# Performance work log

Measured on AMD Instinct MI355X. Metric: run time of the kernel, lower is better.

## Reference

```python
import jax, jax.numpy as jnp
import numpy as np
import math


def setup_inputs() -> dict:
    key = jax.random.key(0)
    kq, kk, kv = jax.random.split(key, 3)
    B, N, H = 4, 4096, 128
    return {
        "q": jax.random.normal(kq, (B, N, H), dtype=jnp.float32),
        "k": jax.random.normal(kk, (B, N, H), dtype=jnp.float32),
        "v": jax.random.normal(kv, (B, N, H), dtype=jnp.float32),
        "block_size": 128,
    }


def reference(q, k, v, block_size):
    # The torch module is an exact online-softmax (flash-attention) tiling of
    # full, unmasked softmax attention: out = softmax(q k^T / sqrt(H)) @ v.
    # The block-wise m/l running updates compute the identical result, so the
    # clean dense form below is the faithful math.
    H = q.shape[-1]
    scale = 1.0 / math.sqrt(H)
    s = jnp.einsum("bnh,bmh->bnm", q, k) * scale  # [B, N, N]
    p = jax.nn.softmax(s, axis=-1)                 # numerically stable softmax
    return jnp.einsum("bnm,bmh->bnh", p, v)
```

## Files before the change

kernel.cpp:

```cpp
#include <hip/hip_runtime.h>

typedef __attribute__((ext_vector_type(4))) float f32x4;
typedef __attribute__((ext_vector_type(8))) short short8;

#define DEVI static __device__ __forceinline__

constexpr int B_ = 4;
constexpr int N_ = 4096;
constexpr int H_ = 128;
constexpr size_t ELEMS = (size_t)B_ * N_ * H_;
constexpr size_t TSB = ELEMS * 2;

constexpr int QT = 128;
constexpr int KVB = 64;
constexpr int NTH = 256;

DEVI unsigned short f2bf(float x) {
  union { float f; unsigned u; } a; a.f = x;
  unsigned u = a.u;
  return (unsigned short)((u + 0x7FFFu + ((u >> 16) & 1u)) >> 16);
}

DEVI int swz(int byteoff, int row) { return byteoff ^ ((row & 7) << 4); }

DEVI void gl_lds16(const void* g, void* l) {
  __builtin_amdgcn_global_load_lds(
      (const __attribute__((address_space(1))) void*)g,
      (__attribute__((address_space(3))) void*)l, 16, 0, 0);
}

__global__ void conv_qk(const float* __restrict__ q, const float* __restrict__ k,
                        unsigned short* __restrict__ qb, unsigned short* __restrict__ kb) {
  const float qscale = 0.08838834764831845f * 1.4426950408889634f;
  size_t i = (size_t)blockIdx.x * blockDim.x + threadIdx.x;
  {
    const float4* s = (const float4*)q + 2 * i;
    float4 a = s[0], b = s[1];
    short8 t;
    t[0] = (short)f2bf(a.x * qscale); t[1] = (short)f2bf(a.y * qscale);
    t[2] = (short)f2bf(a.z * qscale); t[3] = (short)f2bf(a.w * qscale);
    t[4] = (short)f2bf(b.x * qscale); t[5] = (short)f2bf(b.y * qscale);
    t[6] = (short)f2bf(b.z * qscale); t[7] = (short)f2bf(b.w * qscale);
    *(short8*)(qb + i * 8) = t;
  }
  {
    const float4* s = (const float4*)k + 2 * i;
    float4 a = s[0], b = s[1];
    short8 t;
    t[0] = (short)f2bf(a.x); t[1] = (short)f2bf(a.y);
    t[2] = (short)f2bf(a.z); t[3] = (short)f2bf(a.w);
    t[4] = (short)f2bf(b.x); t[5] = (short)f2bf(b.y);
    t[6] = (short)f2bf(b.z); t[7] = (short)f2bf(b.w);
    *(short8*)(kb + i * 8) = t;
  }
}

__global__ void conv_vt(const float* __restrict__ v, unsigned short* __restrict__ vt) {
  __shared__ unsigned short T[64][72];
  const int n0 = blockIdx.x * 64, h0 = blockIdx.y * 64, b = blockIdx.z;
  const int t = threadIdx.x;
  const int c4 = t & 15, r = t >> 4;
#pragma unroll
  for (int i = 0; i < 4; ++i) {
    int n = n0 + r + 16 * i;
    float4 val = *(const float4*)(v + ((size_t)b * N_ + n) * H_ + h0 + 4 * c4);
    T[4 * c4 + 0][r + 16 * i] = f2bf(val.x);
    T[4 * c4 + 1][r + 16 * i] = f2bf(val.y);
    T[4 * c4 + 2][r + 16 * i] = f2bf(val.z);
    T[4 * c4 + 3][r + 16 * i] = f2bf(val.w);
  }
  __syncthreads();
  const int c8 = t & 7, hr = t >> 3;
#pragma unroll
  for (int i = 0; i < 2; ++i) {
    int hl = hr + 32 * i;
    short8 val = *(const short8*)(&T[hl][8 * c8]);
    *(short8*)(vt + ((size_t)b * H_ + h0 + hl) * N_ + n0 + 8 * c8) = val;
  }
}

template <int KS>
__global__ __launch_bounds__(NTH, 2)
void fattn_v4(const unsigned short* __restrict__ qws,
              const unsigned short* __restrict__ kws,
              const unsigned short* __restrict__ vtws,
              float* __restrict__ opart, float* __restrict__ mlpart) {
  constexpr int KVRANGE = N_ / KS;
  constexpr int NST = KVRANGE / KVB;

  __shared__ __align__(16) char smem[73728];
  char* Kb0 = smem;
  char* Vb0 = smem + 32768;

  const int tid = threadIdx.x, wave = tid >> 6, lane = tid & 63;
  const int l15 = lane & 15, l4 = lane >> 4;
  const int b = blockIdx.y, z = blockIdx.z;
  const int qg0 = blockIdx.x * QT + wave * 32;
  const size_t kvz = (size_t)z * KVRANGE;
  const int swzm = (l15 & 7) << 4;
  char* Pw = smem + 65536 + wave * 2048;

  const unsigned short* qp0 = qws + ((size_t)b * N_ + qg0 + l15) * H_;
  short8 qf0[4], qf1[4];
#pragma unroll
  for (int kc = 0; kc < 4; ++kc) {
    qf0[kc] = *(const short8*)(qp0 + 8 * l4 + 32 * kc);
    qf1[kc] = *(const short8*)(qp0 + 16 * H_ + 8 * l4 + 32 * kc);
  }

  f32x4 O0[8], O1[8];
#pragma unroll
  for (int i = 0; i < 8; ++i) { O0[i] = (f32x4){0,0,0,0}; O1[i] = (f32x4){0,0,0,0}; }
  float m0 = -__builtin_inff(), l0 = 0.f, m1 = -__builtin_inff(), l1 = 0.f;

  const char* kbase = (const char*)(kws + ((size_t)b * N_ + kvz) * H_);
  const char* vbase = (const char*)(vtws + (size_t)b * H_ * N_) + kvz * 2;

  auto stage = [&](int buf, int step) {
    const char* kt = kbase + (size_t)step * KVB * H_ * 2;
    char* kd = Kb0 + buf * 16384;
#pragma unroll
    for (int i = 0; i < 4; ++i) {
      int off = (tid + 256 * i) * 16;
      int row = off >> 8, col = off & 255;
      gl_lds16(kt + row * 256 + (col ^ ((row & 7) << 4)), kd + off);
    }
    const char* vt0 = vbase + (size_t)step * KVB * 2;
    char* vd = Vb0 + buf * 16384;
#pragma unroll
    for (int i = 0; i < 4; ++i) {
      int off = (tid + 256 * i) * 16;
      int h = off >> 7, colb = off & 127;
      gl_lds16(vt0 + (size_t)h * (N_ * 2) + (colb ^ ((h & 7) << 4)), vd + off);
    }
  };

  auto softmax_prep = [&](f32x4 (&S)[4], float& m, float& l, f32x4 (&O)[8], short8 (&pf)[2]) {
    float mx = S[0][0];
#pragma unroll
    for (int ct = 0; ct < 4; ++ct)
#pragma unroll
      for (int r = 0; r < 4; ++r) mx = fmaxf(mx, S[ct][r]);
    mx = fmaxf(mx, __shfl_xor(mx, 16));
    mx = fmaxf(mx, __shfl_xor(mx, 32));
    float mi = fmaxf(m, mx);
    float alpha = __builtin_amdgcn_exp2f(m - mi);
    m = mi;
    float rs = 0.f;
    uint2 pk[4];
#pragma unroll
    for (int ct = 0; ct < 4; ++ct) {
      float p0 = __builtin_amdgcn_exp2f(S[ct][0] - mi);
      float p1 = __builtin_amdgcn_exp2f(S[ct][1] - mi);
      float p2 = __builtin_amdgcn_exp2f(S[ct][2] - mi);
      float p3 = __builtin_amdgcn_exp2f(S[ct][3] - mi);
      rs += (p0 + p1) + (p2 + p3);
      pk[ct].x = (unsigned)f2bf(p0) | ((unsigned)f2bf(p1) << 16);
      pk[ct].y = (unsigned)f2bf(p2) | ((unsigned)f2bf(p3) << 16);
    }
    rs += __shfl_xor(rs, 16);
    rs += __shfl_xor(rs, 32);
    l = l * alpha + rs;
#pragma unroll
    for (int i = 0; i < 8; ++i) O[i] = O[i] * alpha;
#pragma unroll
    for (int ct = 0; ct < 4; ++ct)
      *(uint2*)(Pw + ((l15 * 128 + 32 * ct + 8 * l4) ^ swzm)) = pk[ct];
    pf[0] = *(const short8*)(Pw + ((l15 * 128 + 16 * l4) ^ swzm));
    pf[1] = *(const short8*)(Pw + ((l15 * 128 + 16 * l4 + 64) ^ swzm));
  };

  stage(0, 0);
  __syncthreads();
  int cur = 0;

  for (int st = 0; st < NST; ++st) {
    if (st + 1 < NST) stage(cur ^ 1, st + 1);

    const char* Kl = Kb0 + cur * 16384;
    const char* Vl = Vb0 + cur * 16384;

    f32x4 S0[4], S1[4];
#pragma unroll
    for (int ct = 0; ct < 4; ++ct) { S0[ct] = (f32x4){0,0,0,0}; S1[ct] = (f32x4){0,0,0,0}; }
    __builtin_amdgcn_s_setprio(1);
#pragma unroll
    for (int ct = 0; ct < 4; ++ct) {
      int kr = 16 * ct + l15;
#pragma unroll
      for (int kc = 0; kc < 4; ++kc) {
        short8 af = *(const short8*)(Kl + ((kr * 256 + 16 * l4 + 64 * kc) ^ ((kr & 7) << 4)));
        S0[ct] = __builtin_amdgcn_mfma_f32_16x16x32_bf16(af, qf0[kc], S0[ct], 0, 0, 0);
        S1[ct] = __builtin_amdgcn_mfma_f32_16x16x32_bf16(af, qf1[kc], S1[ct], 0, 0, 0);
      }
    }
    __builtin_amdgcn_s_setprio(0);

    short8 pf0[2], pf1[2];
    softmax_prep(S0, m0, l0, O0, pf0);
    softmax_prep(S1, m1, l1, O1, pf1);

    __builtin_amdgcn_s_setprio(1);
#pragma unroll
    for (int ct2 = 0; ct2 < 8; ++ct2) {
      int hr = 16 * ct2 + l15;
#pragma unroll
      for (int kc2 = 0; kc2 < 2; ++kc2) {
        short8 vf = *(const short8*)(Vl + ((hr * 128 + 16 * l4 + 64 * kc2) ^ ((hr & 7) << 4)));
        O0[ct2] = __builtin_amdgcn_mfma_f32_16x16x32_bf16(vf, pf0[kc2], O0[ct2], 0, 0, 0);
        O1[ct2] = __builtin_amdgcn_mfma_f32_16x16x32_bf16(vf, pf1[kc2], O1[ct2], 0, 0, 0);
      }
    }
    __builtin_amdgcn_s_setprio(0);

    __syncthreads();
    cur ^= 1;
  }

#pragma unroll
  for (int ct2 = 0; ct2 < 8; ++ct2) {
    int q0 = wave * 32 + l15;
    *(f32x4*)(smem + q0 * 512 + ((64 * ct2 + 16 * l4) ^ ((q0 & 7) << 4))) = O0[ct2];
    int q1 = q0 + 16;
    *(f32x4*)(smem + q1 * 512 + ((64 * ct2 + 16 * l4) ^ ((q1 & 7) << 4))) = O1[ct2];
  }
  if (l4 == 0) {
    size_t r0 = ((size_t)z * B_ + b) * N_ + qg0 + l15;
    mlpart[2 * r0] = m0;
    mlpart[2 * r0 + 1] = l0;
    mlpart[2 * (r0 + 16)] = m1;
    mlpart[2 * (r0 + 16) + 1] = l1;
  }
  __syncthreads();
  float* od = opart + (((size_t)z * B_ + b) * N_ + (size_t)blockIdx.x * QT) * H_;
#pragma unroll
  for (int i = 0; i < 16; ++i) {
    int off = (tid + 256 * i) * 16;
    int q = off >> 9, colb = off & 511;
    f32x4 val = *(const f32x4*)(smem + q * 512 + (colb ^ ((q & 7) << 4)));
    *(f32x4*)((char*)od + (size_t)q * 512 + colb) = val;
  }
}

template <int KS>
__global__ void combine_k(const float* __restrict__ opart, const float* __restrict__ mlpart,
                          float* __restrict__ out) {
  const int t = threadIdx.x;
  size_t row = (size_t)blockIdx.x * 8 + (t >> 5);
  int hc = (t & 31) * 4;
  float mz[KS], lz[KS];
  float mi = -__builtin_inff();
#pragma unroll
  for (int z = 0; z < KS; ++z) {
    size_t r = (size_t)z * B_ * N_ + row;
    mz[z] = mlpart[2 * r];
    lz[z] = mlpart[2 * r + 1];
    mi = fmaxf(mi, mz[z]);
  }
  float lsum = 0.f;
  float az[KS];
#pragma unroll
  for (int z = 0; z < KS; ++z) {
    az[z] = __builtin_amdgcn_exp2f(mz[z] - mi);
    lsum += az[z] * lz[z];
  }
  float rinv = 1.f / lsum;
  f32x4 acc = (f32x4){0, 0, 0, 0};
#pragma unroll
  for (int z = 0; z < KS; ++z) {
    f32x4 oz = *(const f32x4*)(opart + (size_t)z * B_ * N_ * H_ + row * H_ + hc);
    acc = acc + oz * (az[z] * rinv);
  }
  *(f32x4*)(out + row * H_ + hc) = acc;
}

constexpr int FB_QTILE = 64;
constexpr int FB_KVSTEP = 128;
constexpr int FB_KVHALF = 64;
constexpr int FB_NTH = 512;
constexpr int FB_NSTEPS = N_ / FB_KVSTEP;

__global__ __launch_bounds__(FB_NTH, 2)
void fattn_fast(const unsigned short* __restrict__ qws,
                const unsigned short* __restrict__ kws,
                const unsigned short* __restrict__ vtws,
                float* __restrict__ out) {
  __shared__ unsigned short Kbuf[2][FB_KVSTEP * H_];
  __shared__ unsigned short Vbuf[2][H_ * FB_KVSTEP];
  __shared__ unsigned short Plds[8][16 * FB_KVHALF];
  __shared__ float MLlds[4][16][2];

  const int tid = threadIdx.x;
  const int wave = tid >> 6;
  const int lane = tid & 63;
  const int l15 = lane & 15;
  const int l4 = lane >> 4;
  const int sub = wave & 3;
  const int grp = wave >> 2;

  const int b = blockIdx.y;
  const int qbase = blockIdx.x * FB_QTILE;

  const unsigned short* qp = qws + ((size_t)b * N_ + qbase + sub * 16 + l15) * H_;
  short8 qfrag[4];
#pragma unroll
  for (int kc = 0; kc < 4; ++kc)
    qfrag[kc] = *(const short8*)(qp + 8 * l4 + 32 * kc);

  f32x4 Oacc[8];
#pragma unroll
  for (int i = 0; i < 8; ++i) Oacc[i] = (f32x4){0.f, 0.f, 0.f, 0.f};
  float mrun[4], lrun[4];
#pragma unroll
  for (int r = 0; r < 4; ++r) { mrun[r] = -__builtin_inff(); lrun[r] = 0.f; }

  const char* kbase = (const char*)(kws + (size_t)b * N_ * H_);
  const char* vbase = (const char*)(vtws + (size_t)b * H_ * N_);
  const int kvbase = grp * FB_KVHALF;
  char* pbase = (char*)Plds[wave];

  auto stage = [&](int buf, int step) {
    const char* ktile = kbase + (size_t)step * FB_KVSTEP * H_ * 2;
#pragma unroll
    for (int i = 0; i < 4; ++i) {
      int chunk = wave * 4 + i;
      int off = chunk * 1024 + lane * 16;
      int row = off >> 8, col = off & 255;
      gl_lds16(ktile + row * 256 + (col ^ ((row & 7) << 4)),
               (char*)Kbuf[buf] + chunk * 1024);
    }
#pragma unroll
    for (int i = 0; i < 4; ++i) {
      int chunk = wave * 4 + i;
      int h = chunk * 4 + (lane >> 4);
      int colb = (lane & 15) * 16;
      gl_lds16(vbase + (size_t)h * (N_ * 2) + (size_t)step * 256 + (colb ^ ((h & 7) << 4)),
               (char*)Vbuf[buf] + chunk * 1024);
    }
  };

  int cur = 0;
  stage(0, 0);
  __syncthreads();

  for (int step = 0; step < FB_NSTEPS; ++step) {
    if (step + 1 < FB_NSTEPS) stage(cur ^ 1, step + 1);

    const char* Kl = (const char*)Kbuf[cur];
    const char* Vl = (const char*)Vbuf[cur];

    f32x4 S[4];
#pragma unroll
    for (int ct = 0; ct < 4; ++ct) S[ct] = (f32x4){0.f, 0.f, 0.f, 0.f};
#pragma unroll
    for (int ct = 0; ct < 4; ++ct) {
      int kvrow = kvbase + ct * 16 + l15;
#pragma unroll
      for (int kc = 0; kc < 4; ++kc) {
        short8 bfrag = *(const short8*)(Kl +
            swz(kvrow * 256 + (8 * l4 + 32 * kc) * 2, kvrow));
        S[ct] = __builtin_amdgcn_mfma_f32_16x16x32_bf16(qfrag[kc], bfrag, S[ct], 0, 0, 0);
      }
    }

    float mnew[4];
#pragma unroll
    for (int r = 0; r < 4; ++r) {
      float mx = fmaxf(fmaxf(S[0][r], S[1][r]), fmaxf(S[2][r], S[3][r]));
      mx = fmaxf(mx, __shfl_xor(mx, 1));
      mx = fmaxf(mx, __shfl_xor(mx, 2));
      mx = fmaxf(mx, __shfl_xor(mx, 4));
      mx = fmaxf(mx, __shfl_xor(mx, 8));
      mnew[r] = mx;
    }
    float alpha[4];
#pragma unroll
    for (int r = 0; r < 4; ++r) {
      float mi = fmaxf(mrun[r], mnew[r]);
      alpha[r] = __builtin_amdgcn_exp2f(mrun[r] - mi);
      mrun[r] = mi;
    }
    float rsum[4] = {0.f, 0.f, 0.f, 0.f};
    unsigned short pb[4][4];
#pragma unroll
    for (int ct = 0; ct < 4; ++ct)
#pragma unroll
      for (int r = 0; r < 4; ++r) {
        float pv = __builtin_amdgcn_exp2f(S[ct][r] - mrun[r]);
        rsum[r] += pv;
        pb[ct][r] = f2bf(pv);
      }
#pragma unroll
    for (int r = 0; r < 4; ++r) {
      float s = rsum[r];
      s += __shfl_xor(s, 1); s += __shfl_xor(s, 2);
      s += __shfl_xor(s, 4); s += __shfl_xor(s, 8);
      lrun[r] = lrun[r] * alpha[r] + s;
    }
#pragma unroll
    for (int ct2 = 0; ct2 < 8; ++ct2)
#pragma unroll
      for (int r = 0; r < 4; ++r) Oacc[ct2][r] *= alpha[r];

#pragma unroll
    for (int ct = 0; ct < 4; ++ct)
#pragma unroll
      for (int r = 0; r < 4; ++r) {
        int qrow = 4 * l4 + r;
        int kv = l15 + 16 * ct;
        *(unsigned short*)(pbase + swz(qrow * 128 + kv * 2, qrow)) = pb[ct][r];
      }

#pragma unroll
    for (int kc2 = 0; kc2 < 2; ++kc2) {
      short8 afrag = *(const short8*)(pbase +
          swz(l15 * 128 + (8 * l4 + 32 * kc2) * 2, l15));
#pragma unroll
      for (int ct2 = 0; ct2 < 8; ++ct2) {
        int h = l15 + 16 * ct2;
        short8 bfrag = *(const short8*)(Vl +
            swz(h * 256 + (kvbase + 8 * l4 + 32 * kc2) * 2, h));
        Oacc[ct2] = __builtin_amdgcn_mfma_f32_16x16x32_bf16(afrag, bfrag, Oacc[ct2], 0, 0, 0);
      }
    }

    __syncthreads();
    cur ^= 1;
  }

  __syncthreads();
  float* mergeO = (float*)Kbuf;
  if (grp == 1) {
#pragma unroll
    for (int ct2 = 0; ct2 < 8; ++ct2)
#pragma unroll
      for (int r = 0; r < 4; ++r) {
        int qrow = 4 * l4 + r, h = l15 + 16 * ct2;
        mergeO[(sub * 16 + qrow) * H_ + h] = Oacc[ct2][r];
      }
    if (l15 == 0) {
#pragma unroll
      for (int r = 0; r < 4; ++r) {
        int qrow = 4 * l4 + r;
        MLlds[sub][qrow][0] = mrun[r];
        MLlds[sub][qrow][1] = lrun[r];
      }
    }
  }
  __syncthreads();
  if (grp == 0) {
    float aA[4], aB[4], rl[4];
#pragma unroll
    for (int r = 0; r < 4; ++r) {
      int qrow = 4 * l4 + r;
      float mB = MLlds[sub][qrow][0], lB = MLlds[sub][qrow][1];
      float mi = fmaxf(mrun[r], mB);
      aA[r] = __builtin_amdgcn_exp2f(mrun[r] - mi);
      aB[r] = __builtin_amdgcn_exp2f(mB - mi);
      rl[r] = 1.f / (lrun[r] * aA[r] + lB * aB[r]);
    }
    float* outp = out + ((size_t)b * N_ + qbase + sub * 16) * H_;
#pragma unroll
    for (int ct2 = 0; ct2 < 8; ++ct2)
#pragma unroll
      for (int r = 0; r < 4; ++r) {
        int qrow = 4 * l4 + r, h = l15 + 16 * ct2;
        float ob = mergeO[(sub * 16 + qrow) * H_ + h];
        outp[(size_t)qrow * H_ + h] = (Oacc[ct2][r] * aA[r] + ob * aB[r]) * rl[r];
      }
  }
}

extern "C" void kernel_launch(void* const* d_in, const int* in_sizes, int n_in,
                              void* d_out, int out_size, void* d_ws, size_t ws_size,
                              hipStream_t stream) {
  const float* q = (const float*)d_in[0];
  const float* k = (const float*)d_in[1];
  const float* v = (const float*)d_in[2];
  float* out = (float*)d_out;

  auto need = [](int ks) {
    return 3 * TSB + (size_t)ks * ELEMS * 4 + (size_t)ks * B_ * N_ * 2 * 4;
  };

  if (ws_size >= need(4)) {
    unsigned short* qb = (unsigned short*)d_ws;
    unsigned short* kb = qb + ELEMS;
    unsigned short* vt = kb + ELEMS;
    float* opart = (float*)((char*)d_ws + 3 * TSB);
    float* mlpart = opart + (size_t)4 * ELEMS;
    conv_qk<<<dim3((unsigned)(ELEMS / 8 / 256)), dim3(256), 0, stream>>>(q, k, qb, kb);
    conv_vt<<<dim3(N_ / 64, H_ / 64, B_), dim3(256), 0, stream>>>(v, vt);
    fattn_v4<4><<<dim3(N_ / QT, B_, 4), dim3(NTH), 0, stream>>>(qb, kb, vt, opart, mlpart);
    combine_k<4><<<dim3(B_ * N_ / 8), dim3(256), 0, stream>>>(opart, mlpart, out);
  } else if (ws_size >= need(2)) {
    unsigned short* qb = (unsigned short*)d_ws;
    unsigned short* kb = qb + ELEMS;
    unsigned short* vt = kb + ELEMS;
    float* opart = (float*)((char*)d_ws + 3 * TSB);
    float* mlpart = opart + (size_t)2 * ELEMS;
    conv_qk<<<dim3((unsigned)(ELEMS / 8 / 256)), dim3(256), 0, stream>>>(q, k, qb, kb);
    conv_vt<<<dim3(N_ / 64, H_ / 64, B_), dim3(256), 0, stream>>>(v, vt);
    fattn_v4<2><<<dim3(N_ / QT, B_, 2), dim3(NTH), 0, stream>>>(qb, kb, vt, opart, mlpart);
    combine_k<2><<<dim3(B_ * N_ / 8), dim3(256), 0, stream>>>(opart, mlpart, out);
  } else if (ws_size >= 3 * TSB) {
    unsigned short* qb = (unsigned short*)d_ws;
    unsigned short* kb = qb + ELEMS;
    unsigned short* vt = kb + ELEMS;
    conv_qk<<<dim3((unsigned)(ELEMS / 8 / 256)), dim3(256), 0, stream>>>(q, k, qb, kb);
    conv_vt<<<dim3(N_ / 64, H_ / 64, B_), dim3(256), 0, stream>>>(v, vt);
    fattn_fast<<<dim3(N_ / FB_QTILE, B_), dim3(FB_NTH), 0, stream>>>(qb, kb, vt, out);
  }
}
```

Baseline: 73.54 us.

## Use lazy softmax rescaling, remap grid to 1D for XCD locality, reorder MFMA loops

```diff
diff --git a/kernel.cpp b/kernel.cpp
--- a/kernel.cpp
+++ b/kernel.cpp
@@ -81,7 +81,7 @@
 
 template <int KS>
 __global__ __launch_bounds__(NTH, 2)
-void fattn_v4(const unsigned short* __restrict__ qws,
+void fattn_v5(const unsigned short* __restrict__ qws,
               const unsigned short* __restrict__ kws,
               const unsigned short* __restrict__ vtws,
               float* __restrict__ opart, float* __restrict__ mlpart) {
@@ -94,8 +94,22 @@
 
   const int tid = threadIdx.x, wave = tid >> 6, lane = tid & 63;
   const int l15 = lane & 15, l4 = lane >> 4;
-  const int b = blockIdx.y, z = blockIdx.z;
-  const int qg0 = blockIdx.x * QT + wave * 32;
+
+  const int bid = blockIdx.x;
+  int x, b, z;
+  if (KS == 4) {
+    int pair = (bid & 7) * 2 + ((bid >> 3) & 1);
+    x = bid >> 4;
+    b = pair >> 2;
+    z = pair & 3;
+  } else {
+    int pair = bid & 7;
+    x = bid >> 3;
+    b = pair >> 1;
+    z = pair & 1;
+  }
+
+  const int qg0 = x * QT + wave * 32;
   const size_t kvz = (size_t)z * KVRANGE;
   const int swzm = (l15 & 7) << 4;
   char* Pw = smem + 65536 + wave * 2048;
@@ -111,7 +125,7 @@
   f32x4 O0[8], O1[8];
 #pragma unroll
   for (int i = 0; i < 8; ++i) { O0[i] = (f32x4){0,0,0,0}; O1[i] = (f32x4){0,0,0,0}; }
-  float m0 = -__builtin_inff(), l0 = 0.f, m1 = -__builtin_inff(), l1 = 0.f;
+  float m0 = 0.f, l0 = 0.f, m1 = 0.f, l1 = 0.f;
 
   const char* kbase = (const char*)(kws + ((size_t)b * N_ + kvz) * H_);
   const char* vbase = (const char*)(vtws + (size_t)b * H_ * N_) + kvz * 2;
@@ -136,36 +150,46 @@
   };
 
   auto softmax_prep = [&](f32x4 (&S)[4], float& m, float& l, f32x4 (&O)[8], short8 (&pf)[2]) {
-    float mx = S[0][0];
+    float p[16];
 #pragma unroll
     for (int ct = 0; ct < 4; ++ct)
 #pragma unroll
-      for (int r = 0; r < 4; ++r) mx = fmaxf(mx, S[ct][r]);
+      for (int r = 0; r < 4; ++r)
+        p[4 * ct + r] = __builtin_amdgcn_exp2f(S[ct][r] - m);
+    float a0 = fmaxf(p[0], p[1]), a1 = fmaxf(p[2], p[3]);
+    float a2 = fmaxf(p[4], p[5]), a3 = fmaxf(p[6], p[7]);
+    float a4 = fmaxf(p[8], p[9]), a5 = fmaxf(p[10], p[11]);
+    float a6 = fmaxf(p[12], p[13]), a7 = fmaxf(p[14], p[15]);
+    float b0 = fmaxf(a0, a1), b1 = fmaxf(a2, a3), b2 = fmaxf(a4, a5), b3 = fmaxf(a6, a7);
+    float mx = fmaxf(fmaxf(b0, b1), fmaxf(b2, b3));
     mx = fmaxf(mx, __shfl_xor(mx, 16));
     mx = fmaxf(mx, __shfl_xor(mx, 32));
-    float mi = fmaxf(m, mx);
-    float alpha = __builtin_amdgcn_exp2f(m - mi);
-    m = mi;
-    float rs = 0.f;
-    uint2 pk[4];
-#pragma unroll
-    for (int ct = 0; ct < 4; ++ct) {
-      float p0 = __builtin_amdgcn_exp2f(S[ct][0] - mi);
-      float p1 = __builtin_amdgcn_exp2f(S[ct][1] - mi);
-      float p2 = __builtin_amdgcn_exp2f(S[ct][2] - mi);
-      float p3 = __builtin_amdgcn_exp2f(S[ct][3] - mi);
-      rs += (p0 + p1) + (p2 + p3);
-      pk[ct].x = (unsigned)f2bf(p0) | ((unsigned)f2bf(p1) << 16);
-      pk[ct].y = (unsigned)f2bf(p2) | ((unsigned)f2bf(p3) << 16);
-    }
+    float s0 = (p[0] + p[1]) + (p[2] + p[3]);
+    float s1 = (p[4] + p[5]) + (p[6] + p[7]);
+    float s2 = (p[8] + p[9]) + (p[10] + p[11]);
+    float s3 = (p[12] + p[13]) + (p[14] + p[15]);
+    float rs = (s0 + s1) + (s2 + s3);
     rs += __shfl_xor(rs, 16);
     rs += __shfl_xor(rs, 32);
-    l = l * alpha + rs;
-#pragma unroll
-    for (int i = 0; i < 8; ++i) O[i] = O[i] * alpha;
-#pragma unroll
-    for (int ct = 0; ct < 4; ++ct)
-      *(uint2*)(Pw + ((l15 * 128 + 32 * ct + 8 * l4) ^ swzm)) = pk[ct];
+    if (__builtin_expect(!__all(mx <= 256.f), 0)) {
+      float sc = fmaxf(mx, 1.f);
+      float ai = 1.f / sc;
+      m += __builtin_amdgcn_logf(sc);
+      l = (l + rs) * ai;
+#pragma unroll
+      for (int i = 0; i < 16; ++i) p[i] *= ai;
+#pragma unroll
+      for (int i = 0; i < 8; ++i) O[i] = O[i] * ai;
+    } else {
+      l += rs;
+    }
+#pragma unroll
+    for (int ct = 0; ct < 4; ++ct) {
+      uint2 pk;
+      pk.x = (unsigned)f2bf(p[4 * ct]) | ((unsigned)f2bf(p[4 * ct + 1]) << 16);
+      pk.y = (unsigned)f2bf(p[4 * ct + 2]) | ((unsigned)f2bf(p[4 * ct + 3]) << 16);
+      *(uint2*)(Pw + ((l15 * 128 + 32 * ct + 8 * l4) ^ swzm)) = pk;
+    }
     pf[0] = *(const short8*)(Pw + ((l15 * 128 + 16 * l4) ^ swzm));
     pf[1] = *(const short8*)(Pw + ((l15 * 128 + 16 * l4 + 64) ^ swzm));
   };
@@ -185,10 +209,10 @@
     for (int ct = 0; ct < 4; ++ct) { S0[ct] = (f32x4){0,0,0,0}; S1[ct] = (f32x4){0,0,0,0}; }
     __builtin_amdgcn_s_setprio(1);
 #pragma unroll
-    for (int ct = 0; ct < 4; ++ct) {
-      int kr = 16 * ct + l15;
-#pragma unroll
-      for (int kc = 0; kc < 4; ++kc) {
+    for (int kc = 0; kc < 4; ++kc) {
+#pragma unroll
+      for (int ct = 0; ct < 4; ++ct) {
+        int kr = 16 * ct + l15;
         short8 af = *(const short8*)(Kl + ((kr * 256 + 16 * l4 + 64 * kc) ^ ((kr & 7) << 4)));
         S0[ct] = __builtin_amdgcn_mfma_f32_16x16x32_bf16(af, qf0[kc], S0[ct], 0, 0, 0);
         S1[ct] = __builtin_amdgcn_mfma_f32_16x16x32_bf16(af, qf1[kc], S1[ct], 0, 0, 0);
@@ -202,10 +226,10 @@
 
     __builtin_amdgcn_s_setprio(1);
 #pragma unroll
-    for (int ct2 = 0; ct2 < 8; ++ct2) {
-      int hr = 16 * ct2 + l15;
-#pragma unroll
-      for (int kc2 = 0; kc2 < 2; ++kc2) {
+    for (int kc2 = 0; kc2 < 2; ++kc2) {
+#pragma unroll
+      for (int ct2 = 0; ct2 < 8; ++ct2) {
+        int hr = 16 * ct2 + l15;
         short8 vf = *(const short8*)(Vl + ((hr * 128 + 16 * l4 + 64 * kc2) ^ ((hr & 7) << 4)));
         O0[ct2] = __builtin_amdgcn_mfma_f32_16x16x32_bf16(vf, pf0[kc2], O0[ct2], 0, 0, 0);
         O1[ct2] = __builtin_amdgcn_mfma_f32_16x16x32_bf16(vf, pf1[kc2], O1[ct2], 0, 0, 0);
@@ -232,7 +256,7 @@
     mlpart[2 * (r0 + 16) + 1] = l1;
   }
   __syncthreads();
-  float* od = opart + (((size_t)z * B_ + b) * N_ + (size_t)blockIdx.x * QT) * H_;
+  float* od = opart + (((size_t)z * B_ + b) * N_ + (size_t)x * QT) * H_;
 #pragma unroll
   for (int i = 0; i < 16; ++i) {
     int off = (tid + 256 * i) * 16;
@@ -491,7 +515,7 @@
     float* mlpart = opart + (size_t)4 * ELEMS;
     conv_qk<<<dim3((unsigned)(ELEMS / 8 / 256)), dim3(256), 0, stream>>>(q, k, qb, kb);
     conv_vt<<<dim3(N_ / 64, H_ / 64, B_), dim3(256), 0, stream>>>(v, vt);
-    fattn_v4<4><<<dim3(N_ / QT, B_, 4), dim3(NTH), 0, stream>>>(qb, kb, vt, opart, mlpart);
+    fattn_v5<4><<<dim3(512), dim3(NTH), 0, stream>>>(qb, kb, vt, opart, mlpart);
     combine_k<4><<<dim3(B_ * N_ / 8), dim3(256), 0, stream>>>(opart, mlpart, out);
   } else if (ws_size >= need(2)) {
     unsigned short* qb = (unsigned short*)d_ws;
@@ -501,7 +525,7 @@
     float* mlpart = opart + (size_t)2 * ELEMS;
     conv_qk<<<dim3((unsigned)(ELEMS / 8 / 256)), dim3(256), 0, stream>>>(q, k, qb, kb);
     conv_vt<<<dim3(N_ / 64, H_ / 64, B_), dim3(256), 0, stream>>>(v, vt);
-    fattn_v4<2><<<dim3(N_ / QT, B_, 2), dim3(NTH), 0, stream>>>(qb, kb, vt, opart, mlpart);
+    fattn_v5<2><<<dim3(256), dim3(NTH), 0, stream>>>(qb, kb, vt, opart, mlpart);
     combine_k<2><<<dim3(B_ * N_ / 8), dim3(256), 0, stream>>>(opart, mlpart, out);
   } else if (ws_size >= 3 * TSB) {
     unsigned short* qb = (unsigned short*)d_ws;
```

Measured after the change: 72.00 us. 2.1% less time.
